# Optimization experiments

Measured on AMD Instinct MI355X. Metric: run time of the kernel, lower is better.

Reference implementation:

```python
import jax, jax.numpy as jnp
import numpy as np

LEVEL_N = [81920, 20480, 5120, 1280, 320]  # faces at div..div-4 (div=6, 20*4^d)
K = 10  # SpherePHD conv kernel taps
W_SHAPES = [(64,3),(64,64),(128,64),(128,128),(256,128),(256,256),(256,256),(512,256),(512,512),(512,512),(512,512),(512,512),(512,512)]
BLOCKS = [[0,1],[2,3],[4,5,6],[7,8,9],[10,11,12]]  # conv indices per VGG block


def setup_inputs() -> dict:
    key = jax.random.key(0)
    ks = iter(jax.random.split(key, 64))
    d = {"x": jax.random.normal(next(ks), (2, 3, LEVEL_N[0]), jnp.float32)}
    for l, n in enumerate(LEVEL_N):
        d[f"conv_t{l}"] = jax.random.randint(next(ks), (n, K), 0, n, jnp.int32)
        d[f"adj_t{l}"] = jax.random.randint(next(ks), (n, 4), 0, n, jnp.int32)
        d[f"pool_t{l}"] = jax.random.randint(next(ks), (n // 4,), 0, n, jnp.int32)
    for i, (o, c) in enumerate(W_SHAPES):
        d[f"w{i}"] = jax.random.normal(next(ks), (o, c, K), jnp.float32) * (1.0 / np.sqrt(c * K))
        d[f"b{i}"] = jnp.zeros((o,), jnp.float32)
    return d


def phd_conv(x, w, b, table):
    # x: [B,C,N], table: [N,K] -> gather neighbors [B,C,N,K], weighted sum, ReLU
    g = x[:, :, table]
    y = jnp.einsum('bcnk,ock->bon', g, w) + b[None, :, None]
    return jax.nn.relu(y)


def phd_maxpool(x, adj, pool):
    # max over adjacent faces, then subsample to parent faces
    m = jnp.max(x[:, :, adj], axis=-1)  # [B,C,N]
    return m[:, :, pool]                # [B,C,N/4]


def reference(x, conv_t0, conv_t1, conv_t2, conv_t3, conv_t4,
              adj_t0, adj_t1, adj_t2, adj_t3, adj_t4,
              pool_t0, pool_t1, pool_t2, pool_t3, pool_t4,
              w0, w1, w2, w3, w4, w5, w6, w7, w8, w9, w10, w11, w12,
              b0, b1, b2, b3, b4, b5, b6, b7, b8, b9, b10, b11, b12):
    conv_ts = [conv_t0, conv_t1, conv_t2, conv_t3, conv_t4]
    adj_ts = [adj_t0, adj_t1, adj_t2, adj_t3, adj_t4]
    pool_ts = [pool_t0, pool_t1, pool_t2, pool_t3, pool_t4]
    ws = [w0, w1, w2, w3, w4, w5, w6, w7, w8, w9, w10, w11, w12]
    bs = [b0, b1, b2, b3, b4, b5, b6, b7, b8, b9, b10, b11, b12]
    h = x
    for lvl, idxs in enumerate(BLOCKS):
        for i in idxs:
            h = phd_conv(h, ws[i], bs[i], conv_ts[lvl])
        h = phd_maxpool(h, adj_ts[lvl], pool_ts[lvl])
    return h  # [2, 512, 80]
```

## Files before the change

### kernel.cpp

```cpp
#include <hip/hip_runtime.h>
#include <stdint.h>

typedef __bf16 bf16;
typedef bf16 bf16x8 __attribute__((ext_vector_type(8)));
typedef float f32x4 __attribute__((ext_vector_type(4)));
typedef unsigned short u16x8 __attribute__((ext_vector_type(8)));

__device__ __forceinline__ void gload_lds16(const bf16* g, bf16* l) {
    __builtin_amdgcn_global_load_lds(
        (const __attribute__((address_space(1))) void*)g,
        (__attribute__((address_space(3))) void*)l, 16, 0, 0);
}

template<int C>
__device__ __forceinline__ void cvt_pair(const float* __restrict__ src,
                                         bf16* __restrict__ dst,
                                         int tp, int base5)
{
    int ocp = tp - base5;
    int oc  = ocp * 2;
    int o   = oc / C;
    int c   = oc & (C - 1);
    const f32x4* s4 = (const f32x4*)(src + (size_t)oc * 10);
    float v[20];
#pragma unroll
    for (int j = 0; j < 5; j++) {
        f32x4 p = s4[j];
#pragma unroll
        for (int e = 0; e < 4; e++) v[4 * j + e] = p[e];
    }
    unsigned short* d = (unsigned short*)(dst + (size_t)base5 * 20
                                              + (size_t)o * 10 * C + c);
#pragma unroll
    for (int k = 0; k < 10; k++) {
        union { bf16 h; unsigned short u; } a, b;
        a.h = (bf16)v[k];
        b.h = (bf16)v[10 + k];
        uint32_t pk = (uint32_t)a.u | ((uint32_t)b.u << 16);
        *(uint32_t*)(d + (size_t)k * C) = pk;
    }
}

__global__ __launch_bounds__(256) void prep_w(
    const float* w1, const float* w2, const float* w3, const float* w4,
    const float* w5, const float* w6, const float* w7, const float* w8,
    const float* w9, const float* w10, const float* w11, const float* w12,
    bf16* __restrict__ dst)
{
    int t = blockIdx.x * 256 + threadIdx.x;
    if (t >= 817152) return;
    if      (t <   2048) cvt_pair< 64>(w1,  dst, t, 0);
    else if (t <   6144) cvt_pair< 64>(w2,  dst, t, 2048);
    else if (t <  14336) cvt_pair<128>(w3,  dst, t, 6144);
    else if (t <  30720) cvt_pair<128>(w4,  dst, t, 14336);
    else if (t <  63488) cvt_pair<256>(w5,  dst, t, 30720);
    else if (t <  96256) cvt_pair<256>(w6,  dst, t, 63488);
    else if (t < 161792) cvt_pair<256>(w7,  dst, t, 96256);
    else if (t < 292864) cvt_pair<512>(w8,  dst, t, 161792);
    else if (t < 423936) cvt_pair<512>(w9,  dst, t, 292864);
    else if (t < 555008) cvt_pair<512>(w10, dst, t, 423936);
    else if (t < 686080) cvt_pair<512>(w11, dst, t, 555008);
    else                 cvt_pair<512>(w12, dst, t, 686080);
}

__global__ __launch_bounds__(256) void conv0_kernel(
    const float* __restrict__ x, const float* __restrict__ w0,
    const float* __restrict__ b0, const int* __restrict__ table,
    bf16* __restrict__ out)
{
    const int N = 81920;
    __shared__ float wls[30][64];
    __shared__ float bls[64];
    int tid = threadIdx.x;
    for (int i = tid; i < 1920; i += 256) {
        int o = i / 30, ck = i - o * 30;
        wls[ck][o] = w0[i];
    }
    if (tid < 64) bls[tid] = b0[tid];
    __syncthreads();

    int p = blockIdx.x * 256 + tid;
    int b = p >= N;
    int n = p - b * N;
    int idx[10];
    const int* trow = table + n * 10;
#pragma unroll
    for (int k = 0; k < 10; k++) idx[k] = trow[k];
    float xv[30];
#pragma unroll
    for (int c = 0; c < 3; c++)
#pragma unroll
        for (int k = 0; k < 10; k++)
            xv[c * 10 + k] = x[(b * 3 + c) * N + idx[k]];

    float acc[64];
#pragma unroll
    for (int o = 0; o < 64; o++) acc[o] = bls[o];
    for (int ck = 0; ck < 30; ck++) {
        float xs = xv[ck];
        const f32x4* wrow = (const f32x4*)(&wls[ck][0]);
#pragma unroll
        for (int o4 = 0; o4 < 16; o4++) {
            f32x4 w4 = wrow[o4];
            acc[o4 * 4 + 0] += xs * w4[0];
            acc[o4 * 4 + 1] += xs * w4[1];
            acc[o4 * 4 + 2] += xs * w4[2];
            acc[o4 * 4 + 3] += xs * w4[3];
        }
    }
    bf16x8 ob[8];
#pragma unroll
    for (int i = 0; i < 8; i++)
#pragma unroll
        for (int e = 0; e < 8; e++)
            ob[i][e] = (bf16)fmaxf(acc[i * 8 + e], 0.0f);
    bf16x8* dst = (bf16x8*)(out + (size_t)p * 64);
#pragma unroll
    for (int i = 0; i < 8; i++) dst[i] = ob[i];
}

struct Frags64 {
    bf16x8 a[4][2];
    bf16x8 b[2][2];
};

__global__ __launch_bounds__(256) void conv_reg64(
    const bf16* __restrict__ in, const bf16* __restrict__ w,
    const float* __restrict__ bias, const int* __restrict__ table,
    bf16* __restrict__ out, int N)
{
    const int tid = threadIdx.x;
    const int lane = tid & 63;
    const int wid = tid >> 6;
    const int l16 = lane & 15, q = lane >> 4;

    const int p0 = blockIdx.x * 128 + wid * 32;

    int nrow[2][10];
#pragma unroll
    for (int tp = 0; tp < 2; tp++) {
        int p = p0 + tp * 16 + l16;
        int b = p >= N;
        int n = p - b * N;
        const int* tr = table + n * 10;
#pragma unroll
        for (int k = 0; k < 10; k++)
            nrow[tp][k] = (b * N + tr[k]) * 64;
    }

    const bf16* wbase[4];
#pragma unroll
    for (int to = 0; to < 4; to++)
        wbase[to] = w + (to * 16 + l16) * 640 + q * 8;
    const bf16* xq = in + q * 8;

    f32x4 acc[4][2];
#pragma unroll
    for (int a = 0; a < 4; a++)
#pragma unroll
        for (int c = 0; c < 2; c++) acc[a][c] = (f32x4){0.f, 0.f, 0.f, 0.f};

    auto loadF = [&](int k, Frags64& F) {
#pragma unroll
        for (int to = 0; to < 4; to++)
#pragma unroll
            for (int ks = 0; ks < 2; ks++)
                F.a[to][ks] = *(const bf16x8*)(wbase[to] + k * 64 + ks * 32);
#pragma unroll
        for (int tp = 0; tp < 2; tp++)
#pragma unroll
            for (int ks = 0; ks < 2; ks++)
                F.b[tp][ks] = *(const bf16x8*)(xq + nrow[tp][k] + ks * 32);
    };
    auto mm = [&](Frags64& F) {
#pragma unroll
        for (int ks = 0; ks < 2; ks++)
#pragma unroll
            for (int to = 0; to < 4; to++)
#pragma unroll
                for (int tp = 0; tp < 2; tp++)
                    acc[to][tp] = __builtin_amdgcn_mfma_f32_16x16x32_bf16(
                        F.a[to][ks], F.b[tp][ks], acc[to][tp], 0, 0, 0);
    };

    Frags64 F0, F1;
    loadF(0, F0);
#pragma unroll
    for (int k = 0; k < 10; k += 2) {
        loadF(k + 1, F1);
        mm(F0);
        if (k + 2 < 10) loadF(k + 2, F0);
        mm(F1);
    }

#pragma unroll
    for (int to = 0; to < 4; ++to) {
        int ob = to * 16 + q * 4;
        f32x4 bv = *(const f32x4*)(bias + ob);
#pragma unroll
        for (int tp = 0; tp < 2; ++tp) {
            int p = p0 + tp * 16 + l16;
            union { ushort4 u4; unsigned short s[4]; } pk;
#pragma unroll
            for (int r = 0; r < 4; r++) {
                float v = fmaxf(acc[to][tp][r] + bv[r], 0.0f);
                union { bf16 h; unsigned short u; } cc;
                cc.h = (bf16)v;
                pk.s[r] = cc.u;
            }
            *(ushort4*)(out + (size_t)p * 64 + ob) = pk.u4;
        }
    }
}

template<int C, int BP, int BO, int WO, int WP>
__global__ __launch_bounds__(256) void conv_p(
    const bf16* __restrict__ in, const bf16* __restrict__ w,
    const float* __restrict__ bias, const int* __restrict__ table,
    bf16* __restrict__ out, float* __restrict__ slab,
    int N, int O, int S, int PO)
{
    constexpr int CH = C / 64;
    constexpr int CHUNKS = CH * 10;
    constexpr int CK = C * 10;
    constexpr int TO = (BO / WO) / 16;
    constexpr int TP = (BP / WP) / 16;
    constexpr int XI = BP / 32;
    constexpr int WI = BO / 32;
    constexpr int LPS = XI + WI;
    static_assert(LPS == 4, "vmcnt literal assumes 4 loads/stage");

    __shared__ bf16 Xs[3][BP][64];
    __shared__ bf16 Ws[3][BO][64];
    __shared__ int rowoff[BP][10];

    const int tid = threadIdx.x;
    const int lane = tid & 63;
    const int wid = tid >> 6;
    const int wo = wid & (WO - 1), wp = wid / WO;
    const int l16 = lane & 15, q = lane >> 4;

    const int p0 = blockIdx.x * BP;
    const int o0 = blockIdx.y * BO;
    const int z = blockIdx.z;

    for (int j = tid; j < BP * 10; j += 256) {
        int pp = j / 10, k = j - pp * 10;
        int p = p0 + pp;
        int b = p >= N;
        int n = p - b * N;
        rowoff[pp][k] = (b * N + table[n * 10 + k]) * C;
    }
    __syncthreads();

    int xsrow[XI], xgseg[XI];
#pragma unroll
    for (int t = 0; t < XI; t++) {
        int row = wid * (BP / 4) + t * 8 + (lane >> 3);
        xsrow[t] = row;
        xgseg[t] = (lane & 7) ^ (row & 7);
    }
    const bf16* wbase[WI];
#pragma unroll
    for (int t = 0; t < WI; t++) {
        int row = wid * (BO / 4) + t * 8 + (lane >> 3);
        int gs = (lane & 7) ^ (row & 7);
        wbase[t] = w + (size_t)(o0 + row) * CK + gs * 8;
    }

    const int per = CHUNKS / S;
    const int c0chunk = z * per;

    auto stage = [&](int chunk, int b3) {
        int k = chunk / CH;
        int cofs = (chunk & (CH - 1)) * 64;
#pragma unroll
        for (int t = 0; t < XI; t++) {
            int ro = rowoff[xsrow[t]][k];
            gload_lds16(in + ro + cofs + xgseg[t] * 8,
                        &Xs[b3][wid * (BP / 4) + t * 8][0]);
        }
#pragma unroll
        for (int t = 0; t < WI; t++)
            gload_lds16(wbase[t] + chunk * 64,
                        &Ws[b3][wid * (BO / 4) + t * 8][0]);
    };

    f32x4 acc[TO][TP];
#pragma unroll
    for (int a = 0; a < TO; a++)
#pragma unroll
        for (int c = 0; c < TP; c++) acc[a][c] = (f32x4){0.f, 0.f, 0.f, 0.f};

    stage(c0chunk, 0);
    stage(c0chunk + 1, 1);

    const int obase = wo * (BO / WO);
    const int pbase = wp * (BP / WP);
    const int arow = obase + l16;
    const int brow = pbase + l16;
    const int sx = l16 & 7;

    int bi = 0, bs = 2;
    for (int i = 0; i < per; i++) {
        asm volatile("s_waitcnt vmcnt(4)" ::: "memory");
        __builtin_amdgcn_s_barrier();
        const bf16* xb = &Xs[bi][0][0];
        const bf16* wb = &Ws[bi][0][0];
#pragma unroll
        for (int ks = 0; ks < 2; ks++) {
            int slot = ((ks * 4 + q) ^ sx) * 8;
            bf16x8 af[TO], bfr[TP];
#pragma unroll
            for (int to = 0; to < TO; to++)
                af[to] = *(const bf16x8*)(wb + (arow + to * 16) * 64 + slot);
#pragma unroll
            for (int tp = 0; tp < TP; tp++)
                bfr[tp] = *(const bf16x8*)(xb + (brow + tp * 16) * 64 + slot);
#pragma unroll
            for (int to = 0; to < TO; to++)
#pragma unroll
                for (int tp = 0; tp < TP; tp++)
                    acc[to][tp] = __builtin_amdgcn_mfma_f32_16x16x32_bf16(
                        af[to], bfr[tp], acc[to][tp], 0, 0, 0);
        }
        int nx = i + 2 < per ? i + 2 : per - 1;
        stage(c0chunk + nx, bs);
        bi = bi == 2 ? 0 : bi + 1;
        bs = bs == 2 ? 0 : bs + 1;
    }

    if (S == 1) {
#pragma unroll
        for (int to = 0; to < TO; ++to) {
            int ob = o0 + obase + to * 16 + q * 4;
            f32x4 bv = *(const f32x4*)(bias + ob);
#pragma unroll
            for (int tp = 0; tp < TP; ++tp) {
                int p = p0 + pbase + tp * 16 + l16;
                union { ushort4 u4; unsigned short s[4]; } pk;
#pragma unroll
                for (int r = 0; r < 4; r++) {
                    float v = fmaxf(acc[to][tp][r] + bv[r], 0.0f);
                    union { bf16 h; unsigned short u; } cc;
                    cc.h = (bf16)v;
                    pk.s[r] = cc.u;
                }
                *(ushort4*)(out + (size_t)p * O + ob) = pk.u4;
            }
        }
    } else {
        float* sb = slab + (size_t)z * PO;
#pragma unroll
        for (int to = 0; to < TO; ++to) {
            int ob = o0 + obase + to * 16 + q * 4;
#pragma unroll
            for (int tp = 0; tp < TP; ++tp) {
                int p = p0 + pbase + tp * 16 + l16;
                *(f32x4*)(sb + (size_t)p * O + ob) = acc[to][tp];
            }
        }
    }
}

__global__ __launch_bounds__(256) void epi_reduce(
    const float* __restrict__ slab, const float* __restrict__ bias,
    bf16* __restrict__ out, int PO, int Omask, int S)
{
    int t4 = (blockIdx.x * 256 + threadIdx.x) * 4;
    if (t4 >= PO) return;
    f32x4 s = *(const f32x4*)(slab + t4);
    for (int zz = 1; zz < S; zz++)
        s += *(const f32x4*)(slab + (size_t)zz * PO + t4);
    int o = t4 & Omask;
    f32x4 bv = *(const f32x4*)(bias + o);
    union { ushort4 u4; unsigned short e[4]; } pk;
#pragma unroll
    for (int r = 0; r < 4; r++) {
        float v = fmaxf(s[r] + bv[r], 0.0f);
        union { bf16 h; unsigned short u; } cc;
        cc.h = (bf16)v;
        pk.e[r] = cc.u;
    }
    *(ushort4*)((unsigned short*)out + t4) = pk.u4;
}

__global__ __launch_bounds__(256) void pool_kernel(
    const bf16* __restrict__ in, const int* __restrict__ adj,
    const int* __restrict__ pool, bf16* __restrict__ out,
    int N, int M, int c8shift)
{
    int t = blockIdx.x * 256 + threadIdx.x;
    int total = M << c8shift;
    if (t >= total) return;
    int cc = t & ((1 << c8shift) - 1);
    int j = t >> c8shift;
    int b = blockIdx.y;
    int C = 8 << c8shift;
    int s = pool[j];
    const int* a = adj + s * 4;
    const unsigned short* inu = (const unsigned short*)in;
    size_t base = (size_t)b * N * C + (size_t)cc * 8;
    u16x8 m = *(const u16x8*)(inu + base + (size_t)a[0] * C);
#pragma unroll
    for (int i = 1; i < 4; i++) {
        u16x8 v = *(const u16x8*)(inu + base + (size_t)a[i] * C);
#pragma unroll
        for (int e = 0; e < 8; e++) m[e] = v[e] > m[e] ? v[e] : m[e];
    }
    *(u16x8*)((unsigned short*)out + ((size_t)b * M + j) * C + (size_t)cc * 8) = m;
}

__global__ __launch_bounds__(256) void final_pool(
    const bf16* __restrict__ in, const int* __restrict__ adj,
    const int* __restrict__ pool, float* __restrict__ out)
{
    int t = blockIdx.x * 256 + threadIdx.x;
    if (t >= 81920) return;
    int j = t % 80;
    int rest = t / 80;
    int c = rest & 511;
    int b = rest >> 9;
    int s = pool[j];
    const int* a = adj + s * 4;
    float m = 0.0f;
#pragma unroll
    for (int i = 0; i < 4; i++) {
        float v = (float)in[((size_t)b * 320 + a[i]) * 512 + c];
        m = fmaxf(m, v);
    }
    out[t] = m;
}

extern "C" void kernel_launch(void* const* d_in, const int* in_sizes, int n_in,
                              void* d_out, int out_size, void* d_ws, size_t ws_size,
                              hipStream_t stream)
{
    const float* x = (const float*)d_in[0];
    const int* convT[5]; const int* adjT[5]; const int* poolT[5];
    for (int l = 0; l < 5; l++) {
        convT[l] = (const int*)d_in[1 + 3 * l];
        adjT[l]  = (const int*)d_in[2 + 3 * l];
        poolT[l] = (const int*)d_in[3 + 3 * l];
    }
    const float* W[13]; const float* Bs[13];
    for (int i = 0; i < 13; i++) {
        W[i]  = (const float*)d_in[16 + 2 * i];
        Bs[i] = (const float*)d_in[17 + 2 * i];
    }

    bf16* wbf   = (bf16*)d_ws;
    bf16* A     = (bf16*)((char*)d_ws + (40u << 20));
    bf16* Bb    = (bf16*)((char*)d_ws + (70u << 20));
    float* slabA = (float*)((char*)d_ws + (100u << 20));
    float* slabB = (float*)((char*)d_ws + (130u << 20));

    static const int woff[13] = {0, 0, 40960, 122880, 286720, 614400, 1269760,
                                 1925120, 3235840, 5857280, 8478720, 11100160, 13721600};

    prep_w<<<dim3(817152 / 256), dim3(256), 0, stream>>>(
        W[1], W[2], W[3], W[4], W[5], W[6], W[7], W[8], W[9], W[10], W[11], W[12], wbf);

    conv0_kernel<<<dim3(640), dim3(256), 0, stream>>>(x, W[0], Bs[0], convT[0], A);

    const int PO3 = 2560 * 512;
    const int PO4 = 640 * 512;

    conv_reg64<<<dim3(1280), dim3(256), 0, stream>>>(
        A, wbf + woff[1], Bs[1], convT[0], Bb, 81920);
    pool_kernel<<<dim3(640, 2), dim3(256), 0, stream>>>(Bb, adjT[0], poolT[0], A, 81920, 20480, 3);
    conv_p<64, 64, 64, 2, 2><<<dim3(640, 2, 1), dim3(256), 0, stream>>>(
        A, wbf + woff[2], Bs[2], convT[1], Bb, nullptr, 20480, 128, 1, 0);
    conv_p<128, 64, 64, 2, 2><<<dim3(640, 2, 1), dim3(256), 0, stream>>>(
        Bb, wbf + woff[3], Bs[3], convT[1], A, nullptr, 20480, 128, 1, 0);
    pool_kernel<<<dim3(320, 2), dim3(256), 0, stream>>>(A, adjT[1], poolT[1], Bb, 20480, 5120, 4);
    conv_p<128, 64, 64, 2, 2><<<dim3(160, 4, 1), dim3(256), 0, stream>>>(
        Bb, wbf + woff[4], Bs[4], convT[2], A, nullptr, 5120, 256, 1, 0);
    conv_p<256, 64, 64, 2, 2><<<dim3(160, 4, 1), dim3(256), 0, stream>>>(
        A, wbf + woff[5], Bs[5], convT[2], Bb, nullptr, 5120, 256, 1, 0);
    conv_p<256, 64, 64, 2, 2><<<dim3(160, 4, 1), dim3(256), 0, stream>>>(
        Bb, wbf + woff[6], Bs[6], convT[2], A, nullptr, 5120, 256, 1, 0);
    pool_kernel<<<dim3(160, 2), dim3(256), 0, stream>>>(A, adjT[2], poolT[2], Bb, 5120, 1280, 5);
    conv_p<256, 64, 64, 2, 2><<<dim3(40, 8, 2), dim3(256), 0, stream>>>(
        Bb, wbf + woff[7], Bs[7], convT[3], nullptr, slabA, 1280, 512, 2, PO3);
    epi_reduce<<<dim3(PO3 / 1024), dim3(256), 0, stream>>>(slabA, Bs[7], A, PO3, 511, 2);
    conv_p<512, 64, 64, 2, 2><<<dim3(40, 8, 2), dim3(256), 0, stream>>>(
        A, wbf + woff[8], Bs[8], convT[3], nullptr, slabB, 1280, 512, 2, PO3);
    epi_reduce<<<dim3(PO3 / 1024), dim3(256), 0, stream>>>(slabB, Bs[8], Bb, PO3, 511, 2);
    conv_p<512, 64, 64, 2, 2><<<dim3(40, 8, 2), dim3(256), 0, stream>>>(
        Bb, wbf + woff[9], Bs[9], convT[3], nullptr, slabA, 1280, 512, 2, PO3);
    epi_reduce<<<dim3(PO3 / 1024), dim3(256), 0, stream>>>(slabA, Bs[9], A, PO3, 511, 2);
    pool_kernel<<<dim3(80, 2), dim3(256), 0, stream>>>(A, adjT[3], poolT[3], Bb, 1280, 320, 6);
    conv_p<512, 64, 64, 2, 2><<<dim3(10, 8, 8), dim3(256), 0, stream>>>(
        Bb, wbf + woff[10], Bs[10], convT[4], nullptr, slabA, 320, 512, 8, PO4);
    epi_reduce<<<dim3(PO4 / 1024), dim3(256), 0, stream>>>(slabA, Bs[10], A, PO4, 511, 8);
    conv_p<512, 64, 64, 2, 2><<<dim3(10, 8, 8), dim3(256), 0, stream>>>(
        A, wbf + woff[11], Bs[11], convT[4], nullptr, slabB, 320, 512, 8, PO4);
    epi_reduce<<<dim3(PO4 / 1024), dim3(256), 0, stream>>>(slabB, Bs[11], Bb, PO4, 511, 8);
    conv_p<512, 64, 64, 2, 2><<<dim3(10, 8, 8), dim3(256), 0, stream>>>(
        Bb, wbf + woff[12], Bs[12], convT[4], nullptr, slabA, 320, 512, 8, PO4);
    epi_reduce<<<dim3(PO4 / 1024), dim3(256), 0, stream>>>(slabA, Bs[12], A, PO4, 511, 8);

    final_pool<<<dim3(320), dim3(256), 0, stream>>>(A, adjT[4], poolT[4], (float*)d_out);
}
```

Before: 559.4 us.

## Stage conv64 weights in swizzled LDS and deepen gather prefetch pipeline

The 64-channel conv kernel now copies the full 10x64x64 bf16 weight tensor into shared memory with direct global-to-LDS loads and an XOR swizzle. Each wave then reads its A fragments from LDS instead of re-fetching weights from global memory, which removes redundant weight traffic across waves. The neighbour gathers are prefetched four taps deep with a rotating register buffer, synchronised by a manual vmcnt wait and a barrier. The 80KB LDS footprint and launch_bounds(256,1) limit occupancy to about one block per CU, and the hand-counted vmcnt(16) is fragile.

```diff
diff --git a/kernel.cpp b/kernel.cpp
--- a/kernel.cpp
+++ b/kernel.cpp
@@ -119,20 +119,33 @@
     for (int i = 0; i < 8; i++) dst[i] = ob[i];
 }
 
-struct Frags64 {
-    bf16x8 a[4][2];
-    bf16x8 b[2][2];
-};
-
-__global__ __launch_bounds__(256) void conv_reg64(
+__global__ __launch_bounds__(256, 1) void conv_reg64(
     const bf16* __restrict__ in, const bf16* __restrict__ w,
     const float* __restrict__ bias, const int* __restrict__ table,
     bf16* __restrict__ out, int N)
 {
+    __shared__ bf16 Ws[10][64][64];
+
     const int tid = threadIdx.x;
     const int lane = tid & 63;
     const int wid = tid >> 6;
     const int l16 = lane & 15, q = lane >> 4;
+    const int sx = l16 & 7;
+
+    {
+        int lrow8 = lane >> 3;
+        int lseg  = lane & 7;
+#pragma unroll
+        for (int t = 0; t < 20; t++) {
+            int u = wid * 20 + t;
+            int k = u >> 3;
+            int rb = u & 7;
+            int row = rb * 8 + lrow8;
+            int gs = lseg ^ (row & 7);
+            gload_lds16(w + (size_t)row * 640 + k * 64 + gs * 8,
+                        &Ws[k][rb * 8][0]);
+        }
+    }
 
     const int p0 = blockIdx.x * 128 + wid * 32;
 
@@ -147,11 +160,6 @@
         for (int k = 0; k < 10; k++)
             nrow[tp][k] = (b * N + tr[k]) * 64;
     }
-
-    const bf16* wbase[4];
-#pragma unroll
-    for (int to = 0; to < 4; to++)
-        wbase[to] = w + (to * 16 + l16) * 640 + q * 8;
     const bf16* xq = in + q * 8;
 
     f32x4 acc[4][2];
@@ -160,38 +168,48 @@
 #pragma unroll
         for (int c = 0; c < 2; c++) acc[a][c] = (f32x4){0.f, 0.f, 0.f, 0.f};
 
-    auto loadF = [&](int k, Frags64& F) {
-#pragma unroll
-        for (int to = 0; to < 4; to++)
+    auto loadX = [&](int k, bf16x8 (&B)[2][2]) {
+#pragma unroll
+        for (int tp = 0; tp < 2; tp++)
 #pragma unroll
             for (int ks = 0; ks < 2; ks++)
-                F.a[to][ks] = *(const bf16x8*)(wbase[to] + k * 64 + ks * 32);
-#pragma unroll
-        for (int tp = 0; tp < 2; tp++)
-#pragma unroll
-            for (int ks = 0; ks < 2; ks++)
-                F.b[tp][ks] = *(const bf16x8*)(xq + nrow[tp][k] + ks * 32);
+                B[tp][ks] = *(const bf16x8*)(xq + nrow[tp][k] + ks * 32);
     };
-    auto mm = [&](Frags64& F) {
-#pragma unroll
-        for (int ks = 0; ks < 2; ks++)
+    auto mmc = [&](int k, bf16x8 (&B)[2][2]) {
+#pragma unroll
+        for (int ks = 0; ks < 2; ks++) {
+            bf16x8 af[4];
+#pragma unroll
+            for (int to = 0; to < 4; to++) {
+                int row = to * 16 + l16;
+                int s = (ks * 4 + q) ^ sx;
+                af[to] = *(const bf16x8*)(&Ws[k][row][s * 8]);
+            }
 #pragma unroll
             for (int to = 0; to < 4; to++)
 #pragma unroll
                 for (int tp = 0; tp < 2; tp++)
                     acc[to][tp] = __builtin_amdgcn_mfma_f32_16x16x32_bf16(
-                        F.a[to][ks], F.b[tp][ks], acc[to][tp], 0, 0, 0);
+                        af[to], B[tp][ks], acc[to][tp], 0, 0, 0);
+        }
     };
 
-    Frags64 F0, F1;
-    loadF(0, F0);
-#pragma unroll
-    for (int k = 0; k < 10; k += 2) {
-        loadF(k + 1, F1);
-        mm(F0);
-        if (k + 2 < 10) loadF(k + 2, F0);
-        mm(F1);
-    }
+    bf16x8 B0[2][2], B1[2][2], B2[2][2], B3[2][2];
+    loadX(0, B0); loadX(1, B1); loadX(2, B2); loadX(3, B3);
+
+    asm volatile("s_waitcnt vmcnt(16)" ::: "memory");
+    __builtin_amdgcn_s_barrier();
+
+    mmc(0, B0); loadX(4, B0);
+    mmc(1, B1); loadX(5, B1);
+    mmc(2, B2); loadX(6, B2);
+    mmc(3, B3); loadX(7, B3);
+    mmc(4, B0); loadX(8, B0);
+    mmc(5, B1); loadX(9, B1);
+    mmc(6, B2);
+    mmc(7, B3);
+    mmc(8, B0);
+    mmc(9, B1);
 
 #pragma unroll
     for (int to = 0; to < 4; ++to) {
```

After: 522.0 us. -6.7%, faster.
